# Performance work log

Hardware: AMD Instinct MI355X
Metric: run time of the kernel (lower is better)

## Reference

```python
import jax, jax.numpy as jnp
import numpy as np

HID = 1024      # hidden_dim (== input_dim, forced by spectral feedback)
LAYERS = 3      # num_layers
OUT = 2500      # output_dim = 50*50
GRID = 50       # spatial grid side
MODES = 32      # kept Fourier modes per side


def setup_inputs() -> dict:
    key = jax.random.key(0)
    ks = jax.random.split(key, 7)
    B = 32
    s = 0.02  # small init so tanh/sigmoid stay in a sane range over 64 steps
    return {
        "x": jax.random.normal(ks[0], (B, 1, HID), jnp.float32),
        "W_ih": jax.random.normal(ks[1], (LAYERS, 3 * HID, HID), jnp.float32) * s,
        "W_hh": jax.random.normal(ks[2], (LAYERS, 3 * HID, HID), jnp.float32) * s,
        "b_ih": jax.random.normal(ks[3], (LAYERS, 3 * HID), jnp.float32) * s,
        "b_hh": jax.random.normal(ks[4], (LAYERS, 3 * HID), jnp.float32) * s,
        "fc_w": jax.random.normal(ks[5], (OUT, HID), jnp.float32) * s,
        "fc_b": jax.random.normal(ks[6], (OUT,), jnp.float32) * s,
        "time_size": 64,
    }


def _gru_cell(x, h, w_ih, w_hh, b_ih, b_hh):
    # PyTorch GRU cell: r,z,n gate ordering in the stacked 3H weight matrices.
    gi = x @ w_ih.T + b_ih            # (B, 3H)
    gh = h @ w_hh.T + b_hh            # (B, 3H)
    i_r, i_z, i_n = jnp.split(gi, 3, axis=-1)
    h_r, h_z, h_n = jnp.split(gh, 3, axis=-1)
    r = jax.nn.sigmoid(i_r + h_r)
    z = jax.nn.sigmoid(i_z + h_z)
    n = jnp.tanh(i_n + r * h_n)
    return (1.0 - z) * n + z * h


def _spectral_crop(out):
    # out: (B, 1, OUT) -> real(fftn) -> fftshift -> center 32x32 crop -> (B,1,1024)
    B = out.shape[0]
    sq = out.reshape(B, 1, GRID, GRID)
    f = jnp.real(jnp.fft.fftn(sq, axes=(2, 3)))
    f = jnp.fft.fftshift(f, axes=(2, 3))
    lo = GRID // 2 - MODES // 2   # 9
    hi = GRID // 2 + MODES // 2   # 41
    return f[:, :, lo:hi, lo:hi].astype(jnp.float32).reshape(B, 1, MODES * MODES)


def reference(x, W_ih, W_hh, b_ih, b_hh, fc_w, fc_b, time_size):
    B = x.shape[0]
    h0 = jnp.zeros((LAYERS, B, HID), x.dtype)

    def step(carry, _):
        xin, h = carry
        inp = xin[:, 0, :]                         # seq len is 1: (B, HID)
        hs = []
        for l in range(LAYERS):                    # fixed small layer loop
            hl = _gru_cell(inp, h[l], W_ih[l], W_hh[l], b_ih[l], b_hh[l])
            hs.append(hl)
            inp = hl
        h_new = jnp.stack(hs, axis=0)              # (LAYERS, B, HID)
        out = (inp @ fc_w.T + fc_b)[:, None, :]    # (B, 1, OUT)
        x_next = _spectral_crop(out)               # (B, 1, HID) spectral feedback
        return (x_next, h_new), out

    (_, _), outputs = jax.lax.scan(step, (x, h0), None, length=int(time_size))
    return outputs  # (time_size, B, 1, OUT)
```

## Files before the change

### kernel.cpp

```cpp
#include <hip/hip_runtime.h>
#include <hip/hip_bf16.h>

typedef __attribute__((ext_vector_type(8))) short bf16x8;
typedef __attribute__((ext_vector_type(4))) float f32x4;

#define HID 1024
#define BATCH 32
#define NACT (BATCH * HID)
#define NWIH (3 * 3 * HID * HID)
#define LSTRIDE (3 * HID * HID)
#define NFC (2500 * HID)
#define WXN (HID * HID)
#define WXIN (3 * HID * HID)
#define G3 (3 * HID)
#define TSTEPS 64
#define NBLK 256
#define NTHR 512
#define FSTRIDE 32

__device__ __forceinline__ f32x4 mfma16(bf16x8 a, bf16x8 b, f32x4 c) {
  return __builtin_amdgcn_mfma_f32_16x16x32_bf16(a, b, c, 0, 0, 0);
}
__device__ __forceinline__ float bfbits2f(unsigned short u) {
  return __uint_as_float(((unsigned int)u) << 16);
}
__device__ __forceinline__ unsigned short f2bf_rn(float v) {
  union { __hip_bfloat16 b; unsigned short s; } cv;
  cv.b = __float2bfloat16(v);
  return cv.s;
}
__device__ __forceinline__ void split3(float v, unsigned short& s0, unsigned short& s1,
                                       unsigned short& s2) {
  s0 = (unsigned short)(__float_as_uint(v) >> 16);
  float r1 = v - bfbits2f(s0);
  s1 = (unsigned short)(__float_as_uint(r1) >> 16);
  float r2 = r1 - bfbits2f(s1);
  s2 = f2bf_rn(r2);
}
__device__ __forceinline__ void split2(float v, unsigned short& s0, unsigned short& s1) {
  s0 = (unsigned short)(__float_as_uint(v) >> 16);
  s1 = f2bf_rn(v - bfbits2f(s0));
}
__device__ __forceinline__ bf16x8 ld_act16(const unsigned short* p) {
  union { unsigned long long u[2]; bf16x8 v; } cv;
  cv.u[0] = __hip_atomic_load((unsigned long long*)p, __ATOMIC_RELAXED, __HIP_MEMORY_SCOPE_AGENT);
  cv.u[1] = __hip_atomic_load((unsigned long long*)p + 1, __ATOMIC_RELAXED, __HIP_MEMORY_SCOPE_AGENT);
  return cv.v;
}
__device__ __forceinline__ float ld_f32(const float* p) {
  return __hip_atomic_load(p, __ATOMIC_RELAXED, __HIP_MEMORY_SCOPE_AGENT);
}
__device__ __forceinline__ void st_f32(float* p, float v) {
  __hip_atomic_store(p, v, __ATOMIC_RELAXED, __HIP_MEMORY_SCOPE_AGENT);
}
__device__ __forceinline__ void pst_plane(unsigned short* plane, int eidx, unsigned short s,
                                          int par) {
  int other = __shfl_xor((int)(unsigned int)s, 1, 64);
  unsigned int packed = ((unsigned int)s) | (((unsigned int)(unsigned short)other) << 16);
  if (!par)
    __hip_atomic_store((unsigned int*)(plane + eidx), packed, __ATOMIC_RELAXED,
                       __HIP_MEMORY_SCOPE_AGENT);
}

__global__ void convert_weights(const float* __restrict__ Wih, const float* __restrict__ Whh,
                                unsigned short* __restrict__ WIHP, unsigned short* __restrict__ WHHP) {
  int i0 = blockIdx.x * blockDim.x + threadIdx.x;
  int st = gridDim.x * blockDim.x;
  for (int i = i0; i < NWIH; i += st) {
    unsigned short a0, a1, a2, b0, b1, b2;
    split3(Wih[i], a0, a1, a2);
    split3(Whh[i], b0, b1, b2);
    WIHP[i] = a0; WIHP[NWIH + i] = a1; WIHP[2 * NWIH + i] = a2;
    WHHP[i] = b0; WHHP[NWIH + i] = b1; WHHP[2 * NWIH + i] = b2;
  }
}

__global__ void convert_fcw(const float* __restrict__ fcw, unsigned short* __restrict__ FCWP) {
  int i0 = blockIdx.x * blockDim.x + threadIdx.x;
  int st = gridDim.x * blockDim.x;
  for (int i = i0; i < NFC; i += st) {
    unsigned short c0, c1;
    split2(fcw[i], c0, c1);
    FCWP[i] = c0; FCWP[NFC + i] = c1;
  }
}

__global__ void k_trig(float* __restrict__ cA, float* __restrict__ sA) {
  int i = blockIdx.x * blockDim.x + threadIdx.x;
  if (i < 32 * 50) {
    int a = i / 50, n = i % 50;
    int ka = (a + 34) % 50;
    int ph = (ka * n) % 50;
    float ang = 6.283185307179586f * (float)ph / 50.0f;
    cA[i] = cosf(ang);
    sA[i] = sinf(ang);
  }
}

__global__ void k_pq(const float* __restrict__ fcw, const float* __restrict__ cA,
                     const float* __restrict__ sA, float* __restrict__ P, float* __restrict__ Q,
                     int k0) {
  int n1 = blockIdx.x;
  int kk = threadIdx.x;
  int k = k0 + kk;
  float accP[32], accQ[32];
#pragma unroll
  for (int c = 0; c < 32; ++c) { accP[c] = 0.f; accQ[c] = 0.f; }
  for (int n2 = 0; n2 < 50; ++n2) {
    float w = fcw[(n1 * 50 + n2) * HID + k];
#pragma unroll
    for (int c = 0; c < 32; ++c) {
      accP[c] = fmaf(w, cA[c * 50 + n2], accP[c]);
      accQ[c] = fmaf(w, sA[c * 50 + n2], accQ[c]);
    }
  }
#pragma unroll
  for (int c = 0; c < 32; ++c) {
    P[(n1 * 32 + c) * 256 + kk] = accP[c];
    Q[(n1 * 32 + c) * 256 + kk] = accQ[c];
  }
}

__global__ void k_wx(const float* __restrict__ P, const float* __restrict__ Q,
                     const float* __restrict__ cA, const float* __restrict__ sA,
                     float* __restrict__ WxF, int k0) {
  int j = blockIdx.x;
  int a = j >> 5, c = j & 31;
  int kk = threadIdx.x;
  float acc = 0.f;
  for (int n1 = 0; n1 < 50; ++n1) {
    int base = (n1 * 32 + c) * 256 + kk;
    acc = fmaf(cA[a * 50 + n1], P[base], acc);
    acc = fmaf(-sA[a * 50 + n1], Q[base], acc);
  }
  WxF[j * HID + k0 + kk] = acc;
}

__global__ void k_transpose(const float* __restrict__ WxF, unsigned short* __restrict__ WXTP) {
  __shared__ float lds[64][65];
  int f0 = blockIdx.x * 64, h0 = blockIdx.y * 64;
  for (int idx = threadIdx.x; idx < 4096; idx += 256) {
    int r = idx >> 6, c = idx & 63;
    lds[r][c] = WxF[(f0 + r) * HID + h0 + c];
  }
  __syncthreads();
  for (int idx = threadIdx.x; idx < 4096; idx += 256) {
    int r = idx >> 6, c = idx & 63;
    unsigned short s0, s1, s2;
    split3(lds[c][r], s0, s1, s2);
    int o = (h0 + r) * HID + f0 + c;
    WXTP[o] = s0; WXTP[WXN + o] = s1; WXTP[2 * WXN + o] = s2;
  }
}

__global__ __launch_bounds__(256) void k_compose(const unsigned short* __restrict__ WIHP,
                                                 const unsigned short* __restrict__ WXTP,
                                                 unsigned short* __restrict__ WXIP) {
  int tid = threadIdx.x;
  int L = tid & 63, ws = tid >> 6;
  int col = L & 15, quad = L >> 4;
  int m0 = blockIdx.y * 64 + ws * 16;
  int jt = blockIdx.x * 64;
  f32x4 acc[4];
#pragma unroll
  for (int s = 0; s < 4; ++s) acc[s] = {0.f, 0.f, 0.f, 0.f};
  for (int kt = 0; kt < 32; ++kt) {
    int k0 = kt * 32 + quad * 8;
    bf16x8 a[3], b[3][4];
#pragma unroll
    for (int p = 0; p < 3; ++p)
      a[p] = *(const bf16x8*)(WIHP + (size_t)p * NWIH + (m0 + col) * HID + k0);
#pragma unroll
    for (int s = 0; s < 4; ++s)
#pragma unroll
      for (int p = 0; p < 3; ++p)
        b[p][s] = *(const bf16x8*)(WXTP + (size_t)p * WXN + (jt + s * 16 + col) * HID + k0);
#pragma unroll
    for (int p = 0; p < 3; ++p)
#pragma unroll
      for (int q = 0; q < 3; ++q)
        if (p + q <= 2)
#pragma unroll
          for (int s = 0; s < 4; ++s) acc[s] = mfma16(a[q], b[p][s], acc[s]);
  }
#pragma unroll
  for (int s = 0; s < 4; ++s) {
    int h = jt + s * 16 + col;
#pragma unroll
    for (int r = 0; r < 4; ++r) {
      int g = m0 + quad * 4 + r;
      unsigned short s0, s1;
      split2(acc[s][r], s0, s1);
      WXIP[(size_t)g * HID + h] = s0;
      WXIP[(size_t)WXIN + (size_t)g * HID + h] = s1;
    }
  }
}

__global__ void k_cx(const float* __restrict__ fcb, const float* __restrict__ cA,
                     const float* __restrict__ sA, float* __restrict__ CXV) {
  int j = blockIdx.x * blockDim.x + threadIdx.x;
  if (j >= HID) return;
  int a = j >> 5, c = j & 31;
  float acc = 0.f;
  for (int n1 = 0; n1 < 50; ++n1)
    for (int n2 = 0; n2 < 50; ++n2)
      acc += fcb[n1 * 50 + n2] * (cA[a * 50 + n1] * cA[c * 50 + n2] - sA[a * 50 + n1] * sA[c * 50 + n2]);
  CXV[j] = acc;
}

__global__ void k_bih0c(const float* __restrict__ b_ih, const float* __restrict__ CXV,
                        const float* __restrict__ Wih, float* __restrict__ BIH0C) {
  __shared__ float red[256];
  int g = blockIdx.x;
  float p = 0.f;
  for (int k = threadIdx.x; k < HID; k += 256) p = fmaf(CXV[k], Wih[(size_t)g * HID + k], p);
  red[threadIdx.x] = p;
  __syncthreads();
  for (int s = 128; s > 0; s >>= 1) {
    if (threadIdx.x < s) red[threadIdx.x] += red[threadIdx.x + s];
    __syncthreads();
  }
  if (threadIdx.x == 0) BIH0C[g] = b_ih[g] + red[0];
}

__global__ void setup_state(const float* __restrict__ x_in, float* __restrict__ H,
                            unsigned short* __restrict__ HBP, unsigned short* __restrict__ XBP,
                            unsigned int* __restrict__ flags, unsigned int* __restrict__ rel) {
  int i0 = blockIdx.x * blockDim.x + threadIdx.x;
  int st = gridDim.x * blockDim.x;
  for (int k = i0; k < NBLK * FSTRIDE; k += st) flags[k] = 0u;
  if (i0 == 0) *rel = 0u;
  for (int k = i0; k < 3 * NACT; k += st) H[k] = 0.0f;
  for (int k = i0; k < 3 * 3 * NACT; k += st) HBP[k] = 0;
  for (int k = i0; k < NACT; k += st) {
    unsigned short s0, s1, s2;
    split3(x_in[k], s0, s1, s2);
    XBP[k] = s0; XBP[NACT + k] = s1; XBP[2 * NACT + k] = s2;
  }
}

__device__ __forceinline__ void gbar(unsigned int* flags, unsigned int* rel, unsigned int e) {
  __syncthreads();
  const int tid = threadIdx.x;
  const int bid = blockIdx.x;
  if (tid == 0)
    __hip_atomic_store(flags + bid * FSTRIDE, e, __ATOMIC_RELAXED, __HIP_MEMORY_SCOPE_AGENT);
  if (bid == 0) {
    if (tid < 64) {
      for (;;) {
        bool ok = true;
#pragma unroll
        for (int i = 0; i < 4; ++i) {
          unsigned int v = __hip_atomic_load(flags + (tid + 64 * i) * FSTRIDE, __ATOMIC_RELAXED,
                                             __HIP_MEMORY_SCOPE_AGENT);
          ok &= (v >= e);
        }
        if (__all(ok)) break;
        __builtin_amdgcn_s_sleep(1);
      }
      if (tid == 0) __hip_atomic_store(rel, e, __ATOMIC_RELAXED, __HIP_MEMORY_SCOPE_AGENT);
    }
  } else if (tid == 0) {
    while (__hip_atomic_load(rel, __ATOMIC_RELAXED, __HIP_MEMORY_SCOPE_AGENT) < e)
      __builtin_amdgcn_s_sleep(1);
  }
  __syncthreads();
}

template <int NWP, int NT>
__device__ __forceinline__ void gemm_nt(const unsigned short* __restrict__ Bp, size_t bplane,
                                        const unsigned short* __restrict__ Ap, int gfbase,
                                        float* smem, f32x4 (&acc)[NT][2]) {
  const int tid = threadIdx.x;
  const int L = tid & 63, w = tid >> 6;
  const int col = L & 15, quad = L >> 4;
#pragma unroll
  for (int n = 0; n < NT; ++n) {
    acc[n][0] = {0.f, 0.f, 0.f, 0.f};
    acc[n][1] = {0.f, 0.f, 0.f, 0.f};
  }
  for (int it = 0; it < 4; ++it) {
    int k0 = w * 128 + it * 32 + quad * 8;
    bf16x8 a[3][2], b[NWP][NT];
#pragma unroll
    for (int mh = 0; mh < 2; ++mh) {
      int r = (mh * 16 + col) * HID + k0;
#pragma unroll
      for (int q = 0; q < 3; ++q) a[q][mh] = ld_act16(Ap + (size_t)q * NACT + r);
    }
#pragma unroll
    for (int n = 0; n < NT; ++n) {
      int rr = (gfbase + n * 16 + col) * HID + k0;
#pragma unroll
      for (int p = 0; p < NWP; ++p) b[p][n] = *(const bf16x8*)(Bp + (size_t)p * bplane + rr);
    }
#pragma unroll
    for (int p = 0; p < NWP; ++p)
#pragma unroll
      for (int q = 0; q < 3; ++q)
        if (p + q <= 2)
#pragma unroll
          for (int n = 0; n < NT; ++n)
#pragma unroll
            for (int mh = 0; mh < 2; ++mh) acc[n][mh] = mfma16(a[q][mh], b[p][n], acc[n][mh]);
  }
  __syncthreads();
  if (w > 0) {
    float* s = smem + ((w - 1) * 64 + L) * (NT * 8);
#pragma unroll
    for (int n = 0; n < NT; ++n) {
      *(f32x4*)(s + n * 8) = acc[n][0];
      *(f32x4*)(s + n * 8 + 4) = acc[n][1];
    }
  }
  __syncthreads();
  if (w == 0) {
#pragma unroll
    for (int sx = 0; sx < 7; ++sx) {
      const float* p = smem + (sx * 64 + L) * (NT * 8);
#pragma unroll
      for (int n = 0; n < NT; ++n) {
        acc[n][0] += *(const f32x4*)(p + n * 8);
        acc[n][1] += *(const f32x4*)(p + n * 8 + 4);
      }
    }
  }
}

__global__ __launch_bounds__(NTHR, 2) void gi0_first(const unsigned short* __restrict__ WIHP,
                                                     const unsigned short* __restrict__ XBP,
                                                     float* __restrict__ GI) {
  __shared__ float smem[3584];
  const int tid = threadIdx.x;
  const int L = tid & 63, w = tid >> 6;
  const int col = L & 15, quad = L >> 4;
  int gf = blockIdx.x * 16;
  f32x4 acc[1][2];
  gemm_nt<3, 1>(WIHP, NWIH, XBP, gf, smem, acc);
  if (w == 0) {
#pragma unroll
    for (int mh = 0; mh < 2; ++mh)
#pragma unroll
      for (int r = 0; r < 4; ++r) {
        int b = mh * 16 + quad * 4 + r;
        st_f32(GI + (size_t)b * G3 + gf + col, acc[0][mh][r]);
      }
  }
}

__global__ __launch_bounds__(NTHR, 2) void rnn_persistent(
    const unsigned short* __restrict__ WIHP, const unsigned short* __restrict__ WHHP,
    const unsigned short* __restrict__ WXIP,
    const float* __restrict__ b_ih, const float* __restrict__ b_hh,
    const float* __restrict__ BIH0C,
    float* __restrict__ H,
    unsigned short* __restrict__ HBP,
    float* __restrict__ GH,
    float* __restrict__ GI,
    unsigned short* __restrict__ HIST0, unsigned short* __restrict__ HIST1,
    unsigned int* __restrict__ FLAGS, unsigned int* __restrict__ REL) {
  __shared__ float smem[10752];
  const int tid = threadIdx.x;
  const int L = tid & 63, w = tid >> 6;
  const int col = L & 15, quad = L >> 4;
  const int bid = blockIdx.x;
  unsigned int ep = 0;

#pragma unroll 1
  for (int t = 0; t < TSTEPS; ++t) {
    {
      int s = bid >> 6;
      int gf = (bid & 63) * 48;
      if (s < 3) {
        f32x4 acc[3][2];
        gemm_nt<3, 3>(WHHP + (size_t)s * LSTRIDE, NWIH, HBP + (size_t)s * 3 * NACT, gf, smem, acc);
        if (w == 0) {
          float* outp = GH + (size_t)s * (32 * G3);
#pragma unroll
          for (int n = 0; n < 3; ++n)
#pragma unroll
            for (int mh = 0; mh < 2; ++mh)
#pragma unroll
              for (int r = 0; r < 4; ++r) {
                int b = mh * 16 + quad * 4 + r;
                st_f32(outp + (size_t)b * G3 + gf + n * 16 + col, acc[n][mh][r]);
              }
        }
      } else if (t > 0) {
        f32x4 acc[3][2];
        gemm_nt<2, 3>(WXIP, WXIN, HBP + (size_t)2 * 3 * NACT, gf, smem, acc);
        if (w == 0) {
#pragma unroll
          for (int n = 0; n < 3; ++n)
#pragma unroll
            for (int mh = 0; mh < 2; ++mh)
#pragma unroll
              for (int r = 0; r < 4; ++r) {
                int b = mh * 16 + quad * 4 + r;
                st_f32(GI + (size_t)b * G3 + gf + n * 16 + col, acc[n][mh][r]);
              }
        }
      }
    }
    gbar(FLAGS, REL, ++ep);

#pragma unroll 1
    for (int l = 0; l < 3; ++l) {
      if (bid < 64) {
        int jt = bid * 16;
        int b = tid >> 4, jj = tid & 15, j = jt + jj;
        const float* bi_base = (l == 0) ? ((t == 0) ? b_ih : BIH0C) : (b_ih + l * G3);
        const float* bh_base = b_hh + l * G3;
        float gi[3], gh[3];
#pragma unroll
        for (int g = 0; g < 3; ++g) {
          gi[g] = ld_f32(GI + (size_t)b * G3 + g * HID + j);
          gh[g] = ld_f32(GH + (size_t)l * (32 * G3) + (size_t)b * G3 + g * HID + j);
        }
        float ir = gi[0] + bi_base[j];
        float iz = gi[1] + bi_base[HID + j];
        float in_ = gi[2] + bi_base[2 * HID + j];
        float hr = gh[0] + bh_base[j];
        float hz = gh[1] + bh_base[HID + j];
        float hn = gh[2] + bh_base[2 * HID + j];
        float rr = 1.0f / (1.0f + expf(-(ir + hr)));
        float zz = 1.0f / (1.0f + expf(-(iz + hz)));
        float nn = tanhf(in_ + rr * hn);
        float hold = H[(size_t)l * NACT + b * HID + j];
        float hnew = (1.0f - zz) * nn + zz * hold;
        H[(size_t)l * NACT + b * HID + j] = hnew;
        unsigned short s0, s1, s2;
        split3(hnew, s0, s1, s2);
        int eidx = b * HID + j;
        unsigned short* hb = HBP + (size_t)l * 3 * NACT;
        int par = tid & 1;
        pst_plane(hb, eidx, s0, par);
        pst_plane(hb + NACT, eidx, s1, par);
        pst_plane(hb + 2 * NACT, eidx, s2, par);
        if (l == 2) {
          HIST0[(size_t)(t * BATCH + b) * HID + j] = s0;
          HIST1[(size_t)(t * BATCH + b) * HID + j] = s1;
        }
      }
      gbar(FLAGS, REL, ++ep);

      if (l < 2) {
        if (bid < 192) {
          int gf = bid * 16;
          f32x4 acc[1][2];
          gemm_nt<3, 1>(WIHP + (size_t)(l + 1) * LSTRIDE, NWIH, HBP + (size_t)l * 3 * NACT, gf,
                        smem, acc);
          if (w == 0) {
#pragma unroll
            for (int mh = 0; mh < 2; ++mh)
#pragma unroll
              for (int r = 0; r < 4; ++r) {
                int b = mh * 16 + quad * 4 + r;
                st_f32(GI + (size_t)b * G3 + gf + col, acc[0][mh][r]);
              }
          }
        }
        gbar(FLAGS, REL, ++ep);
      }
    }
  }
}

__global__ __launch_bounds__(256) void final_fc(const unsigned short* __restrict__ H0,
                                                const unsigned short* __restrict__ H1,
                                                const unsigned short* __restrict__ FCWP,
                                                const float* __restrict__ fcb,
                                                float* __restrict__ dout) {
  int tid = threadIdx.x;
  int L = tid & 63, ws = tid >> 6;
  int col = L & 15, quad = L >> 4;
  int m0 = blockIdx.y * 64 + ws * 16;
  int jt = blockIdx.x * 64;
  f32x4 acc[4];
#pragma unroll
  for (int s = 0; s < 4; ++s) acc[s] = {0.f, 0.f, 0.f, 0.f};
  for (int kt = 0; kt < 32; ++kt) {
    int k0 = kt * 32 + quad * 8;
    bf16x8 ah = *(const bf16x8*)(H0 + (size_t)(m0 + col) * HID + k0);
    bf16x8 am = *(const bf16x8*)(H1 + (size_t)(m0 + col) * HID + k0);
    bf16x8 bh[4], bm[4];
#pragma unroll
    for (int s = 0; s < 4; ++s) {
      int jr = jt + s * 16 + col;
      int rc = jr < 2500 ? jr : 2499;
      bh[s] = *(const bf16x8*)(FCWP + (size_t)rc * HID + k0);
      bm[s] = *(const bf16x8*)(FCWP + (size_t)NFC + (size_t)rc * HID + k0);
    }
#pragma unroll
    for (int s = 0; s < 4; ++s) {
      acc[s] = mfma16(ah, bh[s], acc[s]);
      acc[s] = mfma16(ah, bm[s], acc[s]);
      acc[s] = mfma16(am, bh[s], acc[s]);
    }
  }
#pragma unroll
  for (int s = 0; s < 4; ++s) {
    int j = jt + s * 16 + col;
    if (j < 2500) {
      float bias = fcb[j];
#pragma unroll
      for (int r = 0; r < 4; ++r) {
        int R = m0 + quad * 4 + r;
        dout[(size_t)R * 2500 + j] = acc[s][r] + bias;
      }
    }
  }
}

extern "C" void kernel_launch(void* const* d_in, const int* in_sizes, int n_in,
                              void* d_out, int out_size, void* d_ws, size_t ws_size,
                              hipStream_t stream) {
  const float* x_in = (const float*)d_in[0];
  const float* W_ih = (const float*)d_in[1];
  const float* W_hh = (const float*)d_in[2];
  const float* b_ih = (const float*)d_in[3];
  const float* b_hh = (const float*)d_in[4];
  const float* fc_w = (const float*)d_in[5];
  const float* fc_b = (const float*)d_in[6];
  float* dout = (float*)d_out;
  char* ws = (char*)d_ws;

  unsigned short* WIHP = (unsigned short*)(ws + 0);
  unsigned short* WHHP = (unsigned short*)(ws + 56623104);
  unsigned short* WXIP = (unsigned short*)(ws + 113246208);
  unsigned short* FCWP = (unsigned short*)(ws + 113246208);
  float* Pbuf          = (float*)(ws + 125829120);
  float* Qbuf          = (float*)(ws + 127467520);
  float* WxF           = (float*)(ws + 129105920);
  unsigned short* WXTP = (unsigned short*)(ws + 133300224);
  unsigned short* HIST0 = (unsigned short*)(ws + 125829120);
  unsigned short* HIST1 = (unsigned short*)(ws + 130023424);
  float* H             = (float*)(ws + 139591680);
  unsigned short* HBP  = (unsigned short*)(ws + 139984896);
  unsigned short* XBP  = (unsigned short*)(ws + 140574720);
  float* GH            = (float*)(ws + 140771328);
  float* GI            = (float*)(ws + 141950976);
  float* CXV           = (float*)(ws + 142344192);
  float* CA            = (float*)(ws + 142348288);
  float* SA            = (float*)(ws + 142354688);
  float* BIH0C         = (float*)(ws + 142361088);
  unsigned int* FLAGS  = (unsigned int*)(ws + 142373376);
  unsigned int* REL    = (unsigned int*)(ws + 142406144);

  k_trig<<<7, 256, 0, stream>>>(CA, SA);
  for (int k0 = 0; k0 < 1024; k0 += 256) {
    k_pq<<<50, 256, 0, stream>>>(fc_w, CA, SA, Pbuf, Qbuf, k0);
    k_wx<<<1024, 256, 0, stream>>>(Pbuf, Qbuf, CA, SA, WxF, k0);
  }
  k_transpose<<<dim3(16, 16), 256, 0, stream>>>(WxF, WXTP);
  convert_weights<<<2048, 256, 0, stream>>>(W_ih, W_hh, WIHP, WHHP);
  k_compose<<<dim3(16, 48), 256, 0, stream>>>(WIHP, WXTP, WXIP);
  k_cx<<<4, 256, 0, stream>>>(fc_b, CA, SA, CXV);
  k_bih0c<<<3072, 256, 0, stream>>>(b_ih, CXV, W_ih, BIH0C);
  setup_state<<<512, 256, 0, stream>>>(x_in, H, HBP, XBP, FLAGS, REL);
  gi0_first<<<192, NTHR, 0, stream>>>(WIHP, XBP, GI);
  rnn_persistent<<<NBLK, NTHR, 0, stream>>>(WIHP, WHHP, WXIP, b_ih, b_hh, BIH0C, H, HBP,
                                            GH, GI, HIST0, HIST1, FLAGS, REL);
  convert_fcw<<<1024, 256, 0, stream>>>(fc_w, FCWP);
  final_fc<<<dim3(40, 32), 256, 0, stream>>>(HIST0, HIST1, FCWP, fc_b, dout);
}
```

Baseline: 5.706 ms.

## Split-K GEMMs across twice the persistent blocks and drop third weight plane

The persistent RNN kernel now runs 512 blocks instead of 256. Each GEMM task is split into two K-halves whose partial sums go to separate GI/GH buffers and are added in the gate update. Separately, the recurrent and input weights are stored as two bf16 planes instead of three, which cuts weight bytes streamed per step but lowers weight precision. The changes aim to raise parallelism and reduce memory traffic, at the cost of a wider grid barrier, extra partial-sum loads and possible accuracy loss.

```diff
diff --git a/kernel.cpp b/kernel.cpp
--- a/kernel.cpp
+++ b/kernel.cpp
@@ -13,8 +13,10 @@
 #define WXN (HID * HID)
 #define WXIN (3 * HID * HID)
 #define G3 (3 * HID)
+#define NGI (32 * G3)
+#define NGH (3 * 32 * G3)
 #define TSTEPS 64
-#define NBLK 256
+#define NBLK 512
 #define NTHR 512
 #define FSTRIDE 32
 
@@ -67,11 +69,11 @@
   int i0 = blockIdx.x * blockDim.x + threadIdx.x;
   int st = gridDim.x * blockDim.x;
   for (int i = i0; i < NWIH; i += st) {
-    unsigned short a0, a1, a2, b0, b1, b2;
-    split3(Wih[i], a0, a1, a2);
-    split3(Whh[i], b0, b1, b2);
-    WIHP[i] = a0; WIHP[NWIH + i] = a1; WIHP[2 * NWIH + i] = a2;
-    WHHP[i] = b0; WHHP[NWIH + i] = b1; WHHP[2 * NWIH + i] = b2;
+    unsigned short a0, a1, b0, b1;
+    split2(Wih[i], a0, a1);
+    split2(Whh[i], b0, b1);
+    WIHP[i] = a0; WIHP[NWIH + i] = a1;
+    WHHP[i] = b0; WHHP[NWIH + i] = b1;
   }
 }
 
@@ -166,10 +168,10 @@
   for (int s = 0; s < 4; ++s) acc[s] = {0.f, 0.f, 0.f, 0.f};
   for (int kt = 0; kt < 32; ++kt) {
     int k0 = kt * 32 + quad * 8;
-    bf16x8 a[3], b[3][4];
-#pragma unroll
-    for (int p = 0; p < 3; ++p)
-      a[p] = *(const bf16x8*)(WIHP + (size_t)p * NWIH + (m0 + col) * HID + k0);
+    bf16x8 a[2], b[3][4];
+#pragma unroll
+    for (int q = 0; q < 2; ++q)
+      a[q] = *(const bf16x8*)(WIHP + (size_t)q * NWIH + (m0 + col) * HID + k0);
 #pragma unroll
     for (int s = 0; s < 4; ++s)
 #pragma unroll
@@ -178,7 +180,7 @@
 #pragma unroll
     for (int p = 0; p < 3; ++p)
 #pragma unroll
-      for (int q = 0; q < 3; ++q)
+      for (int q = 0; q < 2; ++q)
         if (p + q <= 2)
 #pragma unroll
           for (int s = 0; s < 4; ++s) acc[s] = mfma16(a[q], b[p][s], acc[s]);
@@ -251,7 +253,7 @@
       for (;;) {
         bool ok = true;
 #pragma unroll
-        for (int i = 0; i < 4; ++i) {
+        for (int i = 0; i < 8; ++i) {
           unsigned int v = __hip_atomic_load(flags + (tid + 64 * i) * FSTRIDE, __ATOMIC_RELAXED,
                                              __HIP_MEMORY_SCOPE_AGENT);
           ok &= (v >= e);
@@ -268,10 +270,10 @@
   __syncthreads();
 }
 
-template <int NWP, int NT>
-__device__ __forceinline__ void gemm_nt(const unsigned short* __restrict__ Bp, size_t bplane,
-                                        const unsigned short* __restrict__ Ap, int gfbase,
-                                        float* smem, f32x4 (&acc)[NT][2]) {
+template <int NT>
+__device__ __forceinline__ void gemm_half(const unsigned short* __restrict__ Bp, size_t bplane,
+                                          const unsigned short* __restrict__ Ap, int gfbase,
+                                          int koff, float* smem, f32x4 (&acc)[NT][2]) {
   const int tid = threadIdx.x;
   const int L = tid & 63, w = tid >> 6;
   const int col = L & 15, quad = L >> 4;
@@ -280,9 +282,10 @@
     acc[n][0] = {0.f, 0.f, 0.f, 0.f};
     acc[n][1] = {0.f, 0.f, 0.f, 0.f};
   }
-  for (int it = 0; it < 4; ++it) {
-    int k0 = w * 128 + it * 32 + quad * 8;
-    bf16x8 a[3][2], b[NWP][NT];
+#pragma unroll
+  for (int it = 0; it < 2; ++it) {
+    int k0 = koff + w * 64 + it * 32 + quad * 8;
+    bf16x8 a[3][2], b[2][NT];
 #pragma unroll
     for (int mh = 0; mh < 2; ++mh) {
       int r = (mh * 16 + col) * HID + k0;
@@ -293,10 +296,10 @@
     for (int n = 0; n < NT; ++n) {
       int rr = (gfbase + n * 16 + col) * HID + k0;
 #pragma unroll
-      for (int p = 0; p < NWP; ++p) b[p][n] = *(const bf16x8*)(Bp + (size_t)p * bplane + rr);
-    }
-#pragma unroll
-    for (int p = 0; p < NWP; ++p)
+      for (int p = 0; p < 2; ++p) b[p][n] = *(const bf16x8*)(Bp + (size_t)p * bplane + rr);
+    }
+#pragma unroll
+    for (int p = 0; p < 2; ++p)
 #pragma unroll
       for (int q = 0; q < 3; ++q)
         if (p + q <= 2)
@@ -328,28 +331,30 @@
   }
 }
 
-__global__ __launch_bounds__(NTHR, 2) void gi0_first(const unsigned short* __restrict__ WIHP,
+__global__ __launch_bounds__(NTHR, 4) void gi0_first(const unsigned short* __restrict__ WIHP,
                                                      const unsigned short* __restrict__ XBP,
                                                      float* __restrict__ GI) {
   __shared__ float smem[3584];
   const int tid = threadIdx.x;
   const int L = tid & 63, w = tid >> 6;
   const int col = L & 15, quad = L >> 4;
-  int gf = blockIdx.x * 16;
+  int part = blockIdx.x & 1, tile = blockIdx.x >> 1;
+  int gf = tile * 16;
   f32x4 acc[1][2];
-  gemm_nt<3, 1>(WIHP, NWIH, XBP, gf, smem, acc);
+  gemm_half<1>(WIHP, NWIH, XBP, gf, part * 512, smem, acc);
   if (w == 0) {
+    float* outp = GI + (size_t)part * NGI;
 #pragma unroll
     for (int mh = 0; mh < 2; ++mh)
 #pragma unroll
       for (int r = 0; r < 4; ++r) {
         int b = mh * 16 + quad * 4 + r;
-        st_f32(GI + (size_t)b * G3 + gf + col, acc[0][mh][r]);
-      }
-  }
-}
-
-__global__ __launch_bounds__(NTHR, 2) void rnn_persistent(
+        st_f32(outp + (size_t)b * G3 + gf + col, acc[0][mh][r]);
+      }
+  }
+}
+
+__global__ __launch_bounds__(NTHR, 4) void rnn_persistent(
     const unsigned short* __restrict__ WIHP, const unsigned short* __restrict__ WHHP,
     const unsigned short* __restrict__ WXIP,
     const float* __restrict__ b_ih, const float* __restrict__ b_hh,
@@ -370,13 +375,17 @@
 #pragma unroll 1
   for (int t = 0; t < TSTEPS; ++t) {
     {
-      int s = bid >> 6;
-      int gf = (bid & 63) * 48;
-      if (s < 3) {
+      int part = bid & 1;
+      int task = bid >> 1;
+      int koff = part * 512;
+      if (task < 192) {
+        int s = task >> 6;
+        int gf = (task & 63) * 48;
         f32x4 acc[3][2];
-        gemm_nt<3, 3>(WHHP + (size_t)s * LSTRIDE, NWIH, HBP + (size_t)s * 3 * NACT, gf, smem, acc);
+        gemm_half<3>(WHHP + (size_t)s * LSTRIDE, NWIH, HBP + (size_t)s * 3 * NACT, gf, koff,
+                     smem, acc);
         if (w == 0) {
-          float* outp = GH + (size_t)s * (32 * G3);
+          float* outp = GH + (size_t)part * NGH + (size_t)s * (32 * G3);
 #pragma unroll
           for (int n = 0; n < 3; ++n)
 #pragma unroll
@@ -388,9 +397,11 @@
               }
         }
       } else if (t > 0) {
+        int gf = (task - 192) * 48;
         f32x4 acc[3][2];
-        gemm_nt<2, 3>(WXIP, WXIN, HBP + (size_t)2 * 3 * NACT, gf, smem, acc);
+        gemm_half<3>(WXIP, WXIN, HBP + (size_t)2 * 3 * NACT, gf, koff, smem, acc);
         if (w == 0) {
+          float* outp = GI + (size_t)part * NGI;
 #pragma unroll
           for (int n = 0; n < 3; ++n)
 #pragma unroll
@@ -398,7 +409,7 @@
 #pragma unroll
               for (int r = 0; r < 4; ++r) {
                 int b = mh * 16 + quad * 4 + r;
-                st_f32(GI + (size_t)b * G3 + gf + n * 16 + col, acc[n][mh][r]);
+                st_f32(outp + (size_t)b * G3 + gf + n * 16 + col, acc[n][mh][r]);
               }
         }
       }
@@ -415,8 +426,10 @@
         float gi[3], gh[3];
 #pragma unroll
         for (int g = 0; g < 3; ++g) {
-          gi[g] = ld_f32(GI + (size_t)b * G3 + g * HID + j);
-          gh[g] = ld_f32(GH + (size_t)l * (32 * G3) + (size_t)b * G3 + g * HID + j);
+          size_t off = (size_t)b * G3 + g * HID + j;
+          gi[g] = ld_f32(GI + off) + ld_f32(GI + NGI + off);
+          size_t offh = (size_t)l * (32 * G3) + off;
+          gh[g] = ld_f32(GH + offh) + ld_f32(GH + NGH + offh);
         }
         float ir = gi[0] + bi_base[j];
         float iz = gi[1] + bi_base[HID + j];
@@ -446,18 +459,20 @@
       gbar(FLAGS, REL, ++ep);
 
       if (l < 2) {
-        if (bid < 192) {
-          int gf = bid * 16;
+        if (bid < 384) {
+          int part = bid & 1, tile = bid >> 1;
+          int gf = tile * 16;
           f32x4 acc[1][2];
-          gemm_nt<3, 1>(WIHP + (size_t)(l + 1) * LSTRIDE, NWIH, HBP + (size_t)l * 3 * NACT, gf,
-                        smem, acc);
+          gemm_half<1>(WIHP + (size_t)(l + 1) * LSTRIDE, NWIH, HBP + (size_t)l * 3 * NACT, gf,
+                       part * 512, smem, acc);
           if (w == 0) {
+            float* outp = GI + (size_t)part * NGI;
 #pragma unroll
             for (int mh = 0; mh < 2; ++mh)
 #pragma unroll
               for (int r = 0; r < 4; ++r) {
                 int b = mh * 16 + quad * 4 + r;
-                st_f32(GI + (size_t)b * G3 + gf + col, acc[0][mh][r]);
+                st_f32(outp + (size_t)b * G3 + gf + col, acc[0][mh][r]);
               }
           }
         }
@@ -527,26 +542,26 @@
   char* ws = (char*)d_ws;
 
   unsigned short* WIHP = (unsigned short*)(ws + 0);
-  unsigned short* WHHP = (unsigned short*)(ws + 56623104);
-  unsigned short* WXIP = (unsigned short*)(ws + 113246208);
-  unsigned short* FCWP = (unsigned short*)(ws + 113246208);
-  float* Pbuf          = (float*)(ws + 125829120);
-  float* Qbuf          = (float*)(ws + 127467520);
-  float* WxF           = (float*)(ws + 129105920);
-  unsigned short* WXTP = (unsigned short*)(ws + 133300224);
-  unsigned short* HIST0 = (unsigned short*)(ws + 125829120);
-  unsigned short* HIST1 = (unsigned short*)(ws + 130023424);
-  float* H             = (float*)(ws + 139591680);
-  unsigned short* HBP  = (unsigned short*)(ws + 139984896);
-  unsigned short* XBP  = (unsigned short*)(ws + 140574720);
-  float* GH            = (float*)(ws + 140771328);
-  float* GI            = (float*)(ws + 141950976);
-  float* CXV           = (float*)(ws + 142344192);
-  float* CA            = (float*)(ws + 142348288);
-  float* SA            = (float*)(ws + 142354688);
-  float* BIH0C         = (float*)(ws + 142361088);
-  unsigned int* FLAGS  = (unsigned int*)(ws + 142373376);
-  unsigned int* REL    = (unsigned int*)(ws + 142406144);
+  unsigned short* WHHP = (unsigned short*)(ws + 37748736);
+  unsigned short* WXIP = (unsigned short*)(ws + 75497472);
+  unsigned short* FCWP = (unsigned short*)(ws + 75497472);
+  float* Pbuf          = (float*)(ws + 88080384);
+  float* Qbuf          = (float*)(ws + 89718784);
+  float* WxF           = (float*)(ws + 91357184);
+  unsigned short* WXTP = (unsigned short*)(ws + 95551488);
+  unsigned short* HIST0 = (unsigned short*)(ws + 88080384);
+  unsigned short* HIST1 = (unsigned short*)(ws + 92274688);
+  float* H             = (float*)(ws + 101842944);
+  unsigned short* HBP  = (unsigned short*)(ws + 102236160);
+  unsigned short* XBP  = (unsigned short*)(ws + 102825984);
+  float* GH            = (float*)(ws + 103022592);
+  float* GI            = (float*)(ws + 105381888);
+  float* CXV           = (float*)(ws + 106168320);
+  float* CA            = (float*)(ws + 106172416);
+  float* SA            = (float*)(ws + 106178816);
+  float* BIH0C         = (float*)(ws + 106185216);
+  unsigned int* FLAGS  = (unsigned int*)(ws + 106197504);
+  unsigned int* REL    = (unsigned int*)(ws + 106263040);
 
   k_trig<<<7, 256, 0, stream>>>(CA, SA);
   for (int k0 = 0; k0 < 1024; k0 += 256) {
@@ -559,7 +574,7 @@
   k_cx<<<4, 256, 0, stream>>>(fc_b, CA, SA, CXV);
   k_bih0c<<<3072, 256, 0, stream>>>(b_ih, CXV, W_ih, BIH0C);
   setup_state<<<512, 256, 0, stream>>>(x_in, H, HBP, XBP, FLAGS, REL);
-  gi0_first<<<192, NTHR, 0, stream>>>(WIHP, XBP, GI);
+  gi0_first<<<384, NTHR, 0, stream>>>(WIHP, XBP, GI);
   rnn_persistent<<<NBLK, NTHR, 0, stream>>>(WIHP, WHHP, WXIP, b_ih, b_hh, BIH0C, H, HBP,
                                             GH, GI, HIST0, HIST1, FLAGS, REL);
   convert_fcw<<<1024, 256, 0, stream>>>(fc_w, FCWP);
```

New measurement: 6.190 ms. 8.5% more time.
